# Optimization experiments

Measured on AMD Instinct MI355X. Metric: run time of the kernel, lower is better.

## Reference

```python
import jax, jax.numpy as jnp
import numpy as np

N_SRC = 100000
N_TGT = 100000
E = 600000
IN_SRC = 256
IN_TGT = 256
OUT = 128
LEAKY_SLOPE = 0.2


def setup_inputs() -> dict:
    key = jax.random.key(0)
    k0, k1, k2, k3, k4, k5 = jax.random.split(key, 6)
    src = jax.random.normal(k0, (N_SRC, IN_SRC), dtype=jnp.float32)
    tgt = jax.random.normal(k1, (N_TGT, IN_TGT), dtype=jnp.float32)
    # Linear weights stored as [in, out] so forward is x @ W (same math as torch Linear)
    W_src = jax.random.normal(k2, (IN_SRC, OUT), dtype=jnp.float32) * 0.06
    W_tgt = jax.random.normal(k3, (IN_TGT, OUT), dtype=jnp.float32) * 0.06
    a = jax.random.normal(k4, (2 * OUT, 1), dtype=jnp.float32) * 0.1
    edge_index = jax.random.randint(k5, (2, E), 0, N_SRC, dtype=jnp.int64)
    return {"src": src, "tgt": tgt, "W_src": W_src, "W_tgt": W_tgt, "a": a,
            "edge_index": edge_index}


def reference(src, tgt, W_src, W_tgt, a, edge_index):
    out_dim = W_src.shape[1]
    n_src = src.shape[0]
    h_i = src @ W_src  # [N_src, out]
    h_j = tgt @ W_tgt  # [N_tgt, out]
    src_id = edge_index[0]
    tgt_id = edge_index[1]
    # cat([h_i[s], h_j[t]]) @ a == (h_i @ a[:out])[s] + (h_j @ a[out:])[t]
    score_i = h_i @ a[:out_dim, 0]  # [N_src]
    score_j = h_j @ a[out_dim:, 0]  # [N_tgt]
    e = jax.nn.leaky_relu(score_i[src_id] + score_j[tgt_id],
                          negative_slope=LEAKY_SLOPE)  # [E]
    e = jnp.clip(e, -30.0, 30.0)
    exp_e = jnp.exp(e)
    denom = jax.ops.segment_sum(exp_e, src_id, num_segments=n_src)  # [N_src]
    alpha = exp_e / (denom[src_id] + 1e-8)  # [E]  (dropout: eval mode -> identity)
    msg = h_j[tgt_id] * alpha[:, None]  # [E, out]
    out = jax.ops.segment_sum(msg, src_id, num_segments=n_src)  # [N_src, out]
    return jax.nn.elu(out)  # concat=True branch
```

## Files before the change

kernel.cpp:

```cpp
#include <hip/hip_runtime.h>
#include <hip/hip_bf16.h>
#include <math.h>

#define IN_DIM 256
#define OUT_DIM 128
#define LEAKY 0.2f

typedef __attribute__((ext_vector_type(8))) short bf16x8;
typedef __attribute__((ext_vector_type(4))) float f32x4;

__device__ __forceinline__ unsigned short f2bf(float f) {
    union { float f; unsigned int u; } v; v.f = f;
    unsigned int r = v.u + 0x7FFFu + ((v.u >> 16) & 1u);
    return (unsigned short)(r >> 16);
}
__device__ __forceinline__ float bf2f(unsigned int hi16) {
    union { unsigned int u; float f; } v; v.u = hi16 << 16;
    return v.f;
}

__global__ __launch_bounds__(256) void combine_w_kernel(
    const float* __restrict__ W_src, const float* __restrict__ a,
    float* __restrict__ wcomb) {
    int i = blockIdx.x * blockDim.x + threadIdx.x;
    if (i < 256) {
        float s = 0.f;
        #pragma unroll 4
        for (int k = 0; k < OUT_DIM; ++k) s += W_src[i * OUT_DIM + k] * a[k];
        wcomb[i] = s;
    }
}

__global__ __launch_bounds__(256) void wswz_kernel(
    const float* __restrict__ W, unsigned short* __restrict__ Wswz) {
    int idx = blockIdx.x * 256 + threadIdx.x;
    if (idx >= 4096) return;
    int l  = idx & 63;
    int fj = (idx >> 6) & 7;
    int kc = idx >> 9;
    int col = fj * 16 + (l & 15);
    int kb  = kc * 32 + (l >> 4) * 8;
    unsigned int u[4];
    #pragma unroll
    for (int p = 0; p < 4; ++p) {
        unsigned short e0 = f2bf(W[(size_t)(kb + 2 * p + 0) * OUT_DIM + col]);
        unsigned short e1 = f2bf(W[(size_t)(kb + 2 * p + 1) * OUT_DIM + col]);
        u[p] = (unsigned int)e0 | ((unsigned int)e1 << 16);
    }
    *(uint4*)(Wswz + (size_t)idx * 8) = make_uint4(u[0], u[1], u[2], u[3]);
}

__global__ __launch_bounds__(256) void gemv_score_kernel(
    const float* __restrict__ X, const float* __restrict__ w,
    float* __restrict__ score, int M) {
    int wid = (int)((blockIdx.x * (long long)blockDim.x + threadIdx.x) >> 6);
    int lane = threadIdx.x & 63;
    if (wid >= M) return;
    const float4* row = (const float4*)(X + (size_t)wid * IN_DIM);
    float4 x = row[lane];
    float4 wv = ((const float4*)w)[lane];
    float s = x.x * wv.x + x.y * wv.y + x.z * wv.z + x.w * wv.w;
    #pragma unroll
    for (int d = 1; d < 64; d <<= 1) s += __shfl_xor(s, d);
    if (lane == 0) score[wid] = s;
}

__global__ __launch_bounds__(256) void gemm_mfma_kernel(
    const float* __restrict__ A,
    const unsigned short* __restrict__ Wswz,
    const float* __restrict__ a_hi,
    unsigned short* __restrict__ Hb,
    float* __restrict__ score, int M) {
    __shared__ unsigned short As[64 * 256];
    int tid = threadIdx.x;
    int w = tid >> 6;
    int l = tid & 63;
    int bm = blockIdx.x * 64;

    int srow = tid >> 4;
    int kcol = (tid & 15) * 4;

    float aw[8];
    #pragma unroll
    for (int j = 0; j < 8; ++j) aw[j] = a_hi[j * 16 + (l & 15)];

    f32x4 acc[8];
    f32x4 zero = {0.f, 0.f, 0.f, 0.f};
    #pragma unroll
    for (int j = 0; j < 8; ++j) acc[j] = zero;

    float4 pre[16];
    #pragma unroll
    for (int p = 0; p < 4; ++p) {
        int grow = bm + srow + p * 16;
        const float* rp = A + (size_t)(grow < M ? grow : M - 1) * IN_DIM;
        bool ok = grow < M;
        #pragma unroll
        for (int c = 0; c < 4; ++c) {
            float4 v = *(const float4*)(rp + c * 64 + kcol);
            pre[p * 4 + c] = ok ? v : make_float4(0.f, 0.f, 0.f, 0.f);
        }
    }
    #pragma unroll
    for (int p = 0; p < 4; ++p) {
        int row = srow + p * 16;
        #pragma unroll
        for (int c = 0; c < 4; ++c) {
            float4 v = pre[p * 4 + c];
            unsigned int b0 = (unsigned int)f2bf(v.x) | ((unsigned int)f2bf(v.y) << 16);
            unsigned int b1 = (unsigned int)f2bf(v.z) | ((unsigned int)f2bf(v.w) << 16);
            unsigned int byteoff =
                (unsigned int)(row * 512 + (c * 64 + kcol) * 2) ^ ((row & 7) << 4);
            *(uint2*)((char*)As + byteoff) = make_uint2(b0, b1);
        }
    }
    __syncthreads();

    #pragma unroll
    for (int kc = 0; kc < 8; ++kc) {
        int row = w * 16 + (l & 15);
        unsigned int byteoff =
            (unsigned int)(row * 512 + kc * 64 + (l >> 4) * 16) ^ ((row & 7) << 4);
        bf16x8 af = *(const bf16x8*)((const char*)As + byteoff);
        #pragma unroll
        for (int j = 0; j < 8; ++j) {
            bf16x8 bfj = *(const bf16x8*)(Wswz + ((size_t)(kc * 8 + j) * 64 + l) * 8);
            acc[j] = __builtin_amdgcn_mfma_f32_16x16x32_bf16(af, bfj, acc[j], 0, 0, 0);
        }
    }
    #pragma unroll
    for (int r = 0; r < 4; ++r) {
        int row = bm + w * 16 + (l >> 4) * 4 + r;
        if (row < M) {
            float s = 0.f;
            #pragma unroll
            for (int j = 0; j < 8; ++j) {
                float v = acc[j][r];
                Hb[(size_t)row * OUT_DIM + j * 16 + (l & 15)] = f2bf(v);
                s += v * aw[j];
            }
            s += __shfl_xor(s, 1); s += __shfl_xor(s, 2);
            s += __shfl_xor(s, 4); s += __shfl_xor(s, 8);
            if ((l & 15) == 0) score[row] = s;
        }
    }
}

__global__ __launch_bounds__(256) void hist_rank_kernel(
    const int* __restrict__ src_id, int* __restrict__ counts,
    int* __restrict__ rank, int E) {
    int e = blockIdx.x * blockDim.x + threadIdx.x;
    if (e >= E) return;
    rank[e] = atomicAdd(&counts[src_id[e]], 1);
}

__global__ __launch_bounds__(256) void scan1_kernel(
    const int* __restrict__ counts, int* __restrict__ offs,
    int* __restrict__ blockSums, int n) {
    __shared__ int sd[256];
    int b = blockIdx.x, tid = threadIdx.x;
    int base = b * 1024 + tid * 4;
    int v0 = base + 0 < n ? counts[base + 0] : 0;
    int v1 = base + 1 < n ? counts[base + 1] : 0;
    int v2 = base + 2 < n ? counts[base + 2] : 0;
    int v3 = base + 3 < n ? counts[base + 3] : 0;
    int p1 = v0, p2 = v0 + v1, p3 = v0 + v1 + v2;
    int tsum = p3 + v3;
    sd[tid] = tsum;
    __syncthreads();
    #pragma unroll
    for (int off = 1; off < 256; off <<= 1) {
        int t = tid >= off ? sd[tid - off] : 0;
        __syncthreads();
        sd[tid] += t;
        __syncthreads();
    }
    int ex = sd[tid] - tsum;
    if (base + 0 < n) offs[base + 0] = ex;
    if (base + 1 < n) offs[base + 1] = ex + p1;
    if (base + 2 < n) offs[base + 2] = ex + p2;
    if (base + 3 < n) offs[base + 3] = ex + p3;
    if (tid == 255) blockSums[b] = sd[255];
}

__global__ __launch_bounds__(256) void scan2_kernel(
    const int* __restrict__ blockSums, int* __restrict__ blockOffs, int nb) {
    __shared__ int sd[256];
    int tid = threadIdx.x;
    int v = tid < nb ? blockSums[tid] : 0;
    sd[tid] = v;
    __syncthreads();
    #pragma unroll
    for (int off = 1; off < 256; off <<= 1) {
        int t = tid >= off ? sd[tid - off] : 0;
        __syncthreads();
        sd[tid] += t;
        __syncthreads();
    }
    blockOffs[tid] = sd[tid] - v;
}

__global__ __launch_bounds__(256) void scan3_kernel(
    int* __restrict__ offs, const int* __restrict__ blockOffs, int n, int E) {
    int i = blockIdx.x * blockDim.x + threadIdx.x;
    if (i < n) offs[i] += blockOffs[i >> 10];
    if (i == 0) offs[n] = E;
}

__global__ __launch_bounds__(256) void scatter_fused_kernel(
    const int* __restrict__ src_id, const int* __restrict__ tgt_id,
    const float* __restrict__ score_i, const float* __restrict__ score_j,
    const int* __restrict__ offs, const int* __restrict__ rank,
    uint2* __restrict__ pairs, int E) {
    int e = blockIdx.x * blockDim.x + threadIdx.x;
    if (e >= E) return;
    int s = src_id[e], t = tgt_id[e];
    float x = score_i[s] + score_j[t];
    x = x > 0.f ? x : LEAKY * x;
    x = fminf(30.f, fmaxf(-30.f, x));
    float ex = expf(x);
    int p = offs[s] + rank[e];
    pairs[p] = make_uint2((unsigned int)t, __float_as_uint(ex));
}

__global__ __launch_bounds__(256) void agg_kernel(
    const uint2* __restrict__ pairs, const int* __restrict__ offs,
    const unsigned short* __restrict__ hjb, float* __restrict__ out, int N) {
    int node = (int)((blockIdx.x * (long long)blockDim.x + threadIdx.x) >> 6);
    if (node >= N) return;
    int lane = threadIdx.x & 63;
    int q  = lane >> 4;
    int cl = lane & 15;
    int beg = offs[node], end = offs[node + 1];
    int deg = end - beg;
    float den = 0.f;
    float acc[8];
    #pragma unroll
    for (int i = 0; i < 8; ++i) acc[i] = 0.f;

    int iters = (deg + 3) >> 2;
    for (int it = 0; it < iters; ++it) {
        int e = q + 4 * it;
        bool valid = e < deg;
        int idx = beg + (valid ? e : 0);
        uint2 tw = pairs[idx];
        int t = (int)tw.x;
        float wgt = valid ? __uint_as_float(tw.y) : 0.f;
        den += wgt;
        uint4 u = *(const uint4*)(hjb + (size_t)t * OUT_DIM + cl * 8);
        acc[0] += bf2f(u.x & 0xffffu) * wgt;
        acc[1] += bf2f(u.x >> 16) * wgt;
        acc[2] += bf2f(u.y & 0xffffu) * wgt;
        acc[3] += bf2f(u.y >> 16) * wgt;
        acc[4] += bf2f(u.z & 0xffffu) * wgt;
        acc[5] += bf2f(u.z >> 16) * wgt;
        acc[6] += bf2f(u.w & 0xffffu) * wgt;
        acc[7] += bf2f(u.w >> 16) * wgt;
    }
    den += __shfl_xor(den, 16);
    den += __shfl_xor(den, 32);
    float inv = 1.f / (den + 1e-8f);
    #pragma unroll
    for (int i = 0; i < 8; ++i) {
        acc[i] += __shfl_xor(acc[i], 16);
        acc[i] += __shfl_xor(acc[i], 32);
        acc[i] *= inv;
        acc[i] = acc[i] > 0.f ? acc[i] : expm1f(acc[i]);
    }
    if (lane < 16) {
        float4 v0 = make_float4(acc[0], acc[1], acc[2], acc[3]);
        float4 v1 = make_float4(acc[4], acc[5], acc[6], acc[7]);
        *(float4*)(out + (size_t)node * OUT_DIM + cl * 8) = v0;
        *(float4*)(out + (size_t)node * OUT_DIM + cl * 8 + 4) = v1;
    }
}

__global__ __launch_bounds__(256) void edge_pass1_kernel(
    const int* __restrict__ src_id, const int* __restrict__ tgt_id,
    const float* __restrict__ score_i, const float* __restrict__ score_j,
    float* __restrict__ exp_e, float* __restrict__ denom, int E) {
    int e = blockIdx.x * blockDim.x + threadIdx.x;
    if (e >= E) return;
    int s = src_id[e], t = tgt_id[e];
    float x = score_i[s] + score_j[t];
    x = x > 0.f ? x : LEAKY * x;
    x = fminf(30.f, fmaxf(-30.f, x));
    float ex = expf(x);
    exp_e[e] = ex;
    atomicAdd(&denom[s], ex);
}

__global__ __launch_bounds__(256) void edge_pass2_kernel(
    const int* __restrict__ src_id, const int* __restrict__ tgt_id,
    const unsigned short* __restrict__ hjb, const float* __restrict__ exp_e,
    const float* __restrict__ denom, float* __restrict__ out, int E) {
    int idx = blockIdx.x * blockDim.x + threadIdx.x;
    int e = idx >> 6;
    if (e >= E) return;
    int lane = idx & 63;
    int s = src_id[e], t = tgt_id[e];
    float alpha = exp_e[e] / (denom[s] + 1e-8f);
    unsigned int u = *(const unsigned int*)(hjb + (size_t)t * OUT_DIM + lane * 2);
    atomicAdd(out + (size_t)s * OUT_DIM + lane * 2 + 0, bf2f(u & 0xffffu) * alpha);
    atomicAdd(out + (size_t)s * OUT_DIM + lane * 2 + 1, bf2f(u >> 16) * alpha);
}

__global__ __launch_bounds__(256) void elu_kernel(float* __restrict__ out, int n4) {
    int i = blockIdx.x * blockDim.x + threadIdx.x;
    if (i >= n4) return;
    float4 v = ((float4*)out)[i];
    v.x = v.x > 0.f ? v.x : expm1f(v.x);
    v.y = v.y > 0.f ? v.y : expm1f(v.y);
    v.z = v.z > 0.f ? v.z : expm1f(v.z);
    v.w = v.w > 0.f ? v.w : expm1f(v.w);
    ((float4*)out)[i] = v;
}

extern "C" void kernel_launch(void* const* d_in, const int* in_sizes, int n_in,
                              void* d_out, int out_size, void* d_ws, size_t ws_size,
                              hipStream_t stream) {
    const float* src   = (const float*)d_in[0];
    const float* tgt   = (const float*)d_in[1];
    const float* W_src = (const float*)d_in[2];
    const float* W_tgt = (const float*)d_in[3];
    const float* a     = (const float*)d_in[4];
    const int*   edge  = (const int*)d_in[5];

    int N_src = in_sizes[0] / IN_DIM;
    int N_tgt = in_sizes[1] / IN_DIM;
    int E     = in_sizes[5] / 2;
    const int* src_id = edge;
    const int* tgt_id = edge + E;

    float* out = (float*)d_out;

    char* ws = (char*)d_ws;
    size_t off = 0;
    auto alloc = [&](size_t bytes) {
        void* p = ws + off;
        off += (bytes + 255) & ~(size_t)255;
        return p;
    };

    unsigned short* hjb  = (unsigned short*)alloc((size_t)N_tgt * OUT_DIM * 2);
    float* score_i = (float*)alloc((size_t)N_src * 4);
    float* score_j = (float*)alloc((size_t)N_tgt * 4);
    float* wcomb   = (float*)alloc(256 * 4);
    unsigned short* Wswz = (unsigned short*)alloc(4096 * 8 * 2);
    int*   counts    = (int*)alloc((size_t)N_src * 4);
    int*   offs      = (int*)alloc((size_t)(N_src + 1) * 4);
    int*   blockSums = (int*)alloc(256 * 4);
    int*   blockOffs = (int*)alloc(256 * 4);
    float* denom     = (float*)alloc((size_t)N_src * 4);
    float* exp_e     = (float*)alloc((size_t)E * 4);
    size_t fb_need = off;
    int*   rank      = (int*)alloc((size_t)E * 4);
    uint2* pairs     = (uint2*)alloc((size_t)E * 8);
    size_t csr_need = off;
    (void)fb_need;

    bool use_csr = (ws_size >= csr_need);

    combine_w_kernel<<<1, 256, 0, stream>>>(W_src, a, wcomb);
    wswz_kernel<<<16, 256, 0, stream>>>(W_tgt, Wswz);
    gemv_score_kernel<<<(N_src + 3) / 4, 256, 0, stream>>>(src, wcomb, score_i, N_src);
    gemm_mfma_kernel<<<(N_tgt + 63) / 64, 256, 0, stream>>>(
        tgt, Wswz, a + OUT_DIM, hjb, score_j, N_tgt);

    if (use_csr) {
        hipMemsetAsync(counts, 0, (size_t)N_src * sizeof(int), stream);
        hist_rank_kernel<<<(E + 255) / 256, 256, 0, stream>>>(src_id, counts, rank, E);
        int nb = (N_src + 1023) / 1024;
        scan1_kernel<<<nb, 256, 0, stream>>>(counts, offs, blockSums, N_src);
        scan2_kernel<<<1, 256, 0, stream>>>(blockSums, blockOffs, nb);
        scan3_kernel<<<(N_src + 255) / 256, 256, 0, stream>>>(offs, blockOffs, N_src, E);
        scatter_fused_kernel<<<(E + 255) / 256, 256, 0, stream>>>(
            src_id, tgt_id, score_i, score_j, offs, rank, pairs, E);
        agg_kernel<<<(N_src + 3) / 4, 256, 0, stream>>>(
            pairs, offs, hjb, out, N_src);
    } else {
        hipMemsetAsync(out, 0, (size_t)N_src * OUT_DIM * sizeof(float), stream);
        hipMemsetAsync(denom, 0, (size_t)N_src * sizeof(float), stream);
        edge_pass1_kernel<<<(E + 255) / 256, 256, 0, stream>>>(
            src_id, tgt_id, score_i, score_j, exp_e, denom, E);
        edge_pass2_kernel<<<(int)(((long long)E * 64 + 255) / 256), 256, 0, stream>>>(
            src_id, tgt_id, hjb, exp_e, denom, out, E);
        elu_kernel<<<(N_src * OUT_DIM / 4 + 255) / 256, 256, 0, stream>>>(
            out, N_src * OUT_DIM / 4);
    }
}
```

Baseline: 175.2 us.

## Fuse histogram-rank into score GEMV kernel and widen agg lanes to 16 features

Merges the per-edge atomic histogram and rank computation into the src-score GEMV launch: every eighth block does histogram work and the other seven do GEMV rows, removing one kernel launch and letting atomic traffic overlap with streaming reads. The aggregation kernel now has each lane cover 16 output features with two 16-byte loads, so 8 edges are processed in parallel per wavefront instead of 4. This raises per-thread register use and adds one more shuffle-reduction stage. In the fallback path the fused kernel is launched with E=0 so only the GEMV part runs.

```diff
diff --git a/kernel.cpp b/kernel.cpp
--- a/kernel.cpp
+++ b/kernel.cpp
@@ -50,10 +50,20 @@
     *(uint4*)(Wswz + (size_t)idx * 8) = make_uint4(u[0], u[1], u[2], u[3]);
 }
 
-__global__ __launch_bounds__(256) void gemv_score_kernel(
+__global__ __launch_bounds__(256) void gemv_hist_kernel(
     const float* __restrict__ X, const float* __restrict__ w,
-    float* __restrict__ score, int M) {
-    int wid = (int)((blockIdx.x * (long long)blockDim.x + threadIdx.x) >> 6);
+    float* __restrict__ score, int M,
+    const int* __restrict__ src_id, int* __restrict__ counts,
+    int* __restrict__ rank, int E) {
+    int bid = blockIdx.x;
+    int grp = bid >> 3;
+    if ((bid & 7) == 7) {
+        int e = grp * 256 + threadIdx.x;
+        if (e < E) rank[e] = atomicAdd(&counts[src_id[e]], 1);
+        return;
+    }
+    int gemv_id = bid - grp;
+    int wid = gemv_id * 4 + (threadIdx.x >> 6);
     int lane = threadIdx.x & 63;
     if (wid >= M) return;
     const float4* row = (const float4*)(X + (size_t)wid * IN_DIM);
@@ -146,14 +156,6 @@
     }
 }
 
-__global__ __launch_bounds__(256) void hist_rank_kernel(
-    const int* __restrict__ src_id, int* __restrict__ counts,
-    int* __restrict__ rank, int E) {
-    int e = blockIdx.x * blockDim.x + threadIdx.x;
-    if (e >= E) return;
-    rank[e] = atomicAdd(&counts[src_id[e]], 1);
-}
-
 __global__ __launch_bounds__(256) void scan1_kernel(
     const int* __restrict__ counts, int* __restrict__ offs,
     int* __restrict__ blockSums, int n) {
@@ -229,49 +231,54 @@
     int node = (int)((blockIdx.x * (long long)blockDim.x + threadIdx.x) >> 6);
     if (node >= N) return;
     int lane = threadIdx.x & 63;
-    int q  = lane >> 4;
-    int cl = lane & 15;
+    int g  = lane >> 3;
+    int cl = lane & 7;
     int beg = offs[node], end = offs[node + 1];
     int deg = end - beg;
     float den = 0.f;
-    float acc[8];
-    #pragma unroll
-    for (int i = 0; i < 8; ++i) acc[i] = 0.f;
-
-    int iters = (deg + 3) >> 2;
+    float acc[16];
+    #pragma unroll
+    for (int i = 0; i < 16; ++i) acc[i] = 0.f;
+
+    int iters = (deg + 7) >> 3;
     for (int it = 0; it < iters; ++it) {
-        int e = q + 4 * it;
+        int e = g + 8 * it;
         bool valid = e < deg;
         int idx = beg + (valid ? e : 0);
         uint2 tw = pairs[idx];
         int t = (int)tw.x;
         float wgt = valid ? __uint_as_float(tw.y) : 0.f;
         den += wgt;
-        uint4 u = *(const uint4*)(hjb + (size_t)t * OUT_DIM + cl * 8);
-        acc[0] += bf2f(u.x & 0xffffu) * wgt;
-        acc[1] += bf2f(u.x >> 16) * wgt;
-        acc[2] += bf2f(u.y & 0xffffu) * wgt;
-        acc[3] += bf2f(u.y >> 16) * wgt;
-        acc[4] += bf2f(u.z & 0xffffu) * wgt;
-        acc[5] += bf2f(u.z >> 16) * wgt;
-        acc[6] += bf2f(u.w & 0xffffu) * wgt;
-        acc[7] += bf2f(u.w >> 16) * wgt;
-    }
+        const unsigned short* hp = hjb + (size_t)t * OUT_DIM + cl * 16;
+        uint4 u0 = *(const uint4*)(hp);
+        uint4 u1 = *(const uint4*)(hp + 8);
+        acc[0]  += bf2f(u0.x & 0xffffu) * wgt;  acc[1]  += bf2f(u0.x >> 16) * wgt;
+        acc[2]  += bf2f(u0.y & 0xffffu) * wgt;  acc[3]  += bf2f(u0.y >> 16) * wgt;
+        acc[4]  += bf2f(u0.z & 0xffffu) * wgt;  acc[5]  += bf2f(u0.z >> 16) * wgt;
+        acc[6]  += bf2f(u0.w & 0xffffu) * wgt;  acc[7]  += bf2f(u0.w >> 16) * wgt;
+        acc[8]  += bf2f(u1.x & 0xffffu) * wgt;  acc[9]  += bf2f(u1.x >> 16) * wgt;
+        acc[10] += bf2f(u1.y & 0xffffu) * wgt;  acc[11] += bf2f(u1.y >> 16) * wgt;
+        acc[12] += bf2f(u1.z & 0xffffu) * wgt;  acc[13] += bf2f(u1.z >> 16) * wgt;
+        acc[14] += bf2f(u1.w & 0xffffu) * wgt;  acc[15] += bf2f(u1.w >> 16) * wgt;
+    }
+    den += __shfl_xor(den, 8);
     den += __shfl_xor(den, 16);
     den += __shfl_xor(den, 32);
     float inv = 1.f / (den + 1e-8f);
     #pragma unroll
-    for (int i = 0; i < 8; ++i) {
+    for (int i = 0; i < 16; ++i) {
+        acc[i] += __shfl_xor(acc[i], 8);
         acc[i] += __shfl_xor(acc[i], 16);
         acc[i] += __shfl_xor(acc[i], 32);
         acc[i] *= inv;
         acc[i] = acc[i] > 0.f ? acc[i] : expm1f(acc[i]);
     }
-    if (lane < 16) {
-        float4 v0 = make_float4(acc[0], acc[1], acc[2], acc[3]);
-        float4 v1 = make_float4(acc[4], acc[5], acc[6], acc[7]);
-        *(float4*)(out + (size_t)node * OUT_DIM + cl * 8) = v0;
-        *(float4*)(out + (size_t)node * OUT_DIM + cl * 8 + 4) = v1;
+    if (lane < 8) {
+        float* op = out + (size_t)node * OUT_DIM + cl * 16;
+        *(float4*)(op + 0)  = make_float4(acc[0],  acc[1],  acc[2],  acc[3]);
+        *(float4*)(op + 4)  = make_float4(acc[4],  acc[5],  acc[6],  acc[7]);
+        *(float4*)(op + 8)  = make_float4(acc[8],  acc[9],  acc[10], acc[11]);
+        *(float4*)(op + 12) = make_float4(acc[12], acc[13], acc[14], acc[15]);
     }
 }
 
@@ -363,13 +370,17 @@
 
     combine_w_kernel<<<1, 256, 0, stream>>>(W_src, a, wcomb);
     wswz_kernel<<<16, 256, 0, stream>>>(W_tgt, Wswz);
-    gemv_score_kernel<<<(N_src + 3) / 4, 256, 0, stream>>>(src, wcomb, score_i, N_src);
-    gemm_mfma_kernel<<<(N_tgt + 63) / 64, 256, 0, stream>>>(
-        tgt, Wswz, a + OUT_DIM, hjb, score_j, N_tgt);
 
     if (use_csr) {
         hipMemsetAsync(counts, 0, (size_t)N_src * sizeof(int), stream);
-        hist_rank_kernel<<<(E + 255) / 256, 256, 0, stream>>>(src_id, counts, rank, E);
+        int gemvBlocks = (N_src + 3) / 4;
+        int histBlocks = (E + 255) / 256;
+        int g7 = (gemvBlocks + 6) / 7;
+        int T = 8 * (histBlocks > g7 ? histBlocks : g7);
+        gemv_hist_kernel<<<T, 256, 0, stream>>>(
+            src, wcomb, score_i, N_src, src_id, counts, rank, E);
+        gemm_mfma_kernel<<<(N_tgt + 63) / 64, 256, 0, stream>>>(
+            tgt, Wswz, a + OUT_DIM, hjb, score_j, N_tgt);
         int nb = (N_src + 1023) / 1024;
         scan1_kernel<<<nb, 256, 0, stream>>>(counts, offs, blockSums, N_src);
         scan2_kernel<<<1, 256, 0, stream>>>(blockSums, blockOffs, nb);
@@ -379,6 +390,11 @@
         agg_kernel<<<(N_src + 3) / 4, 256, 0, stream>>>(
             pairs, offs, hjb, out, N_src);
     } else {
+        int gemvBlocks = (N_src + 3) / 4;
+        gemv_hist_kernel<<<8 * ((gemvBlocks + 6) / 7), 256, 0, stream>>>(
+            src, wcomb, score_i, N_src, src_id, counts, rank, 0);
+        gemm_mfma_kernel<<<(N_tgt + 63) / 64, 256, 0, stream>>>(
+            tgt, Wswz, a + OUT_DIM, hjb, score_j, N_tgt);
         hipMemsetAsync(out, 0, (size_t)N_src * OUT_DIM * sizeof(float), stream);
         hipMemsetAsync(denom, 0, (size_t)N_src * sizeof(float), stream);
         edge_pass1_kernel<<<(E + 255) / 256, 256, 0, stream>>>(
```

Result: slower. 193.5 us (+10.4%).

## Merge prep kernels, fuse histogram into GEMV, fold scan3 into consumers

Applied to the files above, without the earlier changes.

Combines the weight-combine and weight-swizzle kernels into one launch. Interleaves the edge histogram/rank atomics into the source GEMV grid (one block in eight) so both memory-bound passes share a launch. Drops the scan3 pass by adding the per-1024 block offset when offsets are read in the scatter and aggregate kernels. This removes several launches and a pass over the offsets array, at the cost of extra index arithmetic and a more complex block mapping.

```diff
diff --git a/kernel.cpp b/kernel.cpp
--- a/kernel.cpp
+++ b/kernel.cpp
@@ -19,22 +19,19 @@
     return v.f;
 }
 
-__global__ __launch_bounds__(256) void combine_w_kernel(
-    const float* __restrict__ W_src, const float* __restrict__ a,
-    float* __restrict__ wcomb) {
-    int i = blockIdx.x * blockDim.x + threadIdx.x;
-    if (i < 256) {
+__global__ __launch_bounds__(256) void prep_kernel(
+    const float* __restrict__ W_src, const float* __restrict__ W_tgt,
+    const float* __restrict__ a, float* __restrict__ wcomb,
+    unsigned short* __restrict__ Wswz) {
+    if (blockIdx.x == 16) {
+        int i = threadIdx.x;
         float s = 0.f;
         #pragma unroll 4
         for (int k = 0; k < OUT_DIM; ++k) s += W_src[i * OUT_DIM + k] * a[k];
         wcomb[i] = s;
-    }
-}
-
-__global__ __launch_bounds__(256) void wswz_kernel(
-    const float* __restrict__ W, unsigned short* __restrict__ Wswz) {
+        return;
+    }
     int idx = blockIdx.x * 256 + threadIdx.x;
-    if (idx >= 4096) return;
     int l  = idx & 63;
     int fj = (idx >> 6) & 7;
     int kc = idx >> 9;
@@ -43,17 +40,27 @@
     unsigned int u[4];
     #pragma unroll
     for (int p = 0; p < 4; ++p) {
-        unsigned short e0 = f2bf(W[(size_t)(kb + 2 * p + 0) * OUT_DIM + col]);
-        unsigned short e1 = f2bf(W[(size_t)(kb + 2 * p + 1) * OUT_DIM + col]);
+        unsigned short e0 = f2bf(W_tgt[(size_t)(kb + 2 * p + 0) * OUT_DIM + col]);
+        unsigned short e1 = f2bf(W_tgt[(size_t)(kb + 2 * p + 1) * OUT_DIM + col]);
         u[p] = (unsigned int)e0 | ((unsigned int)e1 << 16);
     }
     *(uint4*)(Wswz + (size_t)idx * 8) = make_uint4(u[0], u[1], u[2], u[3]);
 }
 
-__global__ __launch_bounds__(256) void gemv_score_kernel(
+__global__ __launch_bounds__(256) void gemv_hist_kernel(
     const float* __restrict__ X, const float* __restrict__ w,
-    float* __restrict__ score, int M) {
-    int wid = (int)((blockIdx.x * (long long)blockDim.x + threadIdx.x) >> 6);
+    float* __restrict__ score, int M,
+    const int* __restrict__ src_id, int* __restrict__ counts,
+    int* __restrict__ rank, int E) {
+    int bid = blockIdx.x;
+    int grp = bid >> 3;
+    if ((bid & 7) == 7) {
+        int e = grp * 256 + threadIdx.x;
+        if (e < E) rank[e] = atomicAdd(&counts[src_id[e]], 1);
+        return;
+    }
+    int gemv_id = bid - grp;
+    int wid = gemv_id * 4 + (threadIdx.x >> 6);
     int lane = threadIdx.x & 63;
     if (wid >= M) return;
     const float4* row = (const float4*)(X + (size_t)wid * IN_DIM);
@@ -146,14 +153,6 @@
     }
 }
 
-__global__ __launch_bounds__(256) void hist_rank_kernel(
-    const int* __restrict__ src_id, int* __restrict__ counts,
-    int* __restrict__ rank, int E) {
-    int e = blockIdx.x * blockDim.x + threadIdx.x;
-    if (e >= E) return;
-    rank[e] = atomicAdd(&counts[src_id[e]], 1);
-}
-
 __global__ __launch_bounds__(256) void scan1_kernel(
     const int* __restrict__ counts, int* __restrict__ offs,
     int* __restrict__ blockSums, int n) {
@@ -200,18 +199,11 @@
     blockOffs[tid] = sd[tid] - v;
 }
 
-__global__ __launch_bounds__(256) void scan3_kernel(
-    int* __restrict__ offs, const int* __restrict__ blockOffs, int n, int E) {
-    int i = blockIdx.x * blockDim.x + threadIdx.x;
-    if (i < n) offs[i] += blockOffs[i >> 10];
-    if (i == 0) offs[n] = E;
-}
-
 __global__ __launch_bounds__(256) void scatter_fused_kernel(
     const int* __restrict__ src_id, const int* __restrict__ tgt_id,
     const float* __restrict__ score_i, const float* __restrict__ score_j,
-    const int* __restrict__ offs, const int* __restrict__ rank,
-    uint2* __restrict__ pairs, int E) {
+    const int* __restrict__ offs, const int* __restrict__ blockOffs,
+    const int* __restrict__ rank, uint2* __restrict__ pairs, int E) {
     int e = blockIdx.x * blockDim.x + threadIdx.x;
     if (e >= E) return;
     int s = src_id[e], t = tgt_id[e];
@@ -219,19 +211,21 @@
     x = x > 0.f ? x : LEAKY * x;
     x = fminf(30.f, fmaxf(-30.f, x));
     float ex = expf(x);
-    int p = offs[s] + rank[e];
+    int p = offs[s] + blockOffs[s >> 10] + rank[e];
     pairs[p] = make_uint2((unsigned int)t, __float_as_uint(ex));
 }
 
 __global__ __launch_bounds__(256) void agg_kernel(
     const uint2* __restrict__ pairs, const int* __restrict__ offs,
-    const unsigned short* __restrict__ hjb, float* __restrict__ out, int N) {
+    const int* __restrict__ blockOffs, const unsigned short* __restrict__ hjb,
+    float* __restrict__ out, int N, int E) {
     int node = (int)((blockIdx.x * (long long)blockDim.x + threadIdx.x) >> 6);
     if (node >= N) return;
     int lane = threadIdx.x & 63;
     int q  = lane >> 4;
     int cl = lane & 15;
-    int beg = offs[node], end = offs[node + 1];
+    int beg = offs[node] + blockOffs[node >> 10];
+    int end = (node + 1 < N) ? offs[node + 1] + blockOffs[(node + 1) >> 10] : E;
     int deg = end - beg;
     float den = 0.f;
     float acc[8];
@@ -361,24 +355,31 @@
 
     bool use_csr = (ws_size >= csr_need);
 
-    combine_w_kernel<<<1, 256, 0, stream>>>(W_src, a, wcomb);
-    wswz_kernel<<<16, 256, 0, stream>>>(W_tgt, Wswz);
-    gemv_score_kernel<<<(N_src + 3) / 4, 256, 0, stream>>>(src, wcomb, score_i, N_src);
-    gemm_mfma_kernel<<<(N_tgt + 63) / 64, 256, 0, stream>>>(
-        tgt, Wswz, a + OUT_DIM, hjb, score_j, N_tgt);
+    prep_kernel<<<17, 256, 0, stream>>>(W_src, W_tgt, a, wcomb, Wswz);
 
     if (use_csr) {
         hipMemsetAsync(counts, 0, (size_t)N_src * sizeof(int), stream);
-        hist_rank_kernel<<<(E + 255) / 256, 256, 0, stream>>>(src_id, counts, rank, E);
+        int gemvBlocks = (N_src + 3) / 4;
+        int histBlocks = (E + 255) / 256;
+        int g7 = (gemvBlocks + 6) / 7;
+        int T = 8 * (histBlocks > g7 ? histBlocks : g7);
+        gemv_hist_kernel<<<T, 256, 0, stream>>>(
+            src, wcomb, score_i, N_src, src_id, counts, rank, E);
+        gemm_mfma_kernel<<<(N_tgt + 63) / 64, 256, 0, stream>>>(
+            tgt, Wswz, a + OUT_DIM, hjb, score_j, N_tgt);
         int nb = (N_src + 1023) / 1024;
         scan1_kernel<<<nb, 256, 0, stream>>>(counts, offs, blockSums, N_src);
         scan2_kernel<<<1, 256, 0, stream>>>(blockSums, blockOffs, nb);
-        scan3_kernel<<<(N_src + 255) / 256, 256, 0, stream>>>(offs, blockOffs, N_src, E);
         scatter_fused_kernel<<<(E + 255) / 256, 256, 0, stream>>>(
-            src_id, tgt_id, score_i, score_j, offs, rank, pairs, E);
+            src_id, tgt_id, score_i, score_j, offs, blockOffs, rank, pairs, E);
         agg_kernel<<<(N_src + 3) / 4, 256, 0, stream>>>(
-            pairs, offs, hjb, out, N_src);
+            pairs, offs, blockOffs, hjb, out, N_src, E);
     } else {
+        int gemvBlocks = (N_src + 3) / 4;
+        gemv_hist_kernel<<<8 * ((gemvBlocks + 6) / 7), 256, 0, stream>>>(
+            src, wcomb, score_i, N_src, src_id, counts, rank, 0);
+        gemm_mfma_kernel<<<(N_tgt + 63) / 64, 256, 0, stream>>>(
+            tgt, Wswz, a + OUT_DIM, hjb, score_j, N_tgt);
         hipMemsetAsync(out, 0, (size_t)N_src * OUT_DIM * sizeof(float), stream);
         hipMemsetAsync(denom, 0, (size_t)N_src * sizeof(float), stream);
         edge_pass1_kernel<<<(E + 255) / 256, 256, 0, stream>>>(
```

Result: no change. 172.4 us (-1.6%).
